# Kernel tuning notes

Hardware: AMD Instinct MI355X
Metric: run time of the kernel (lower is better)

The kernel has to match this reference:

```python
import jax, jax.numpy as jnp
import numpy as np

N = 131072          # collocation points per dataset
C_WAVE = 1.0        # wave speed c
DIMS = [2, 256, 256, 256, 256, 1]


def _glorot(k, shape):
    fan_in, fan_out = shape
    std = jnp.sqrt(2.0 / (fan_in + fan_out)).astype(jnp.float32)
    return std * jax.random.normal(k, shape, dtype=jnp.float32)


def setup_inputs() -> dict:
    key = jax.random.key(0)
    ks = jax.random.split(key, 16)
    inp = {}
    for i in range(5):
        inp[f"W{i}"] = _glorot(ks[i], (DIMS[i], DIMS[i + 1]))
        inp[f"b{i}"] = jnp.zeros((DIMS[i + 1],), jnp.float32)
    inp["tx_equation"] = jax.random.uniform(ks[10], (N, 2), dtype=jnp.float32)
    inp["tx_init"] = jax.random.uniform(ks[11], (N, 2), dtype=jnp.float32)
    # initial condition points have t=0 in practice; values don't affect the math pattern
    inp["tx_init"] = inp["tx_init"].at[:, 0].set(0.0)
    inp["tx_bound"] = jax.random.uniform(ks[12], (N, 2), dtype=jnp.float32)
    return inp


def _mlp(params, tx):
    # tanh MLP: (..., 2) -> (..., 1)
    h = tx
    for W, b in params[:-1]:
        h = jnp.tanh(h @ W + b)
    W, b = params[-1]
    return h @ W + b


def reference(W0, b0, W1, b1, W2, b2, W3, b3, W4, b4,
              tx_equation, tx_init, tx_bound):
    params = [(W0, b0), (W1, b1), (W2, b2), (W3, b3), (W4, b4)]

    def u_scalar(tx):  # tx: (2,) -> scalar u(t, x)
        return _mlp(params, tx[None, :])[0, 0]

    # PDE residual: u_tt - c^2 * u_xx via per-point Hessian diagonal (input_diagonal_hessian)
    hess = jax.vmap(jax.hessian(u_scalar))(tx_equation)      # (N, 2, 2)
    u_tt = hess[:, 0, 0]
    u_xx = hess[:, 1, 1]
    pde_residual = (u_tt - (C_WAVE ** 2) * u_xx)[:, None]     # (N, 1)

    # Initial conditions: u and du/dt (input_gradient)
    u_init, g = jax.vmap(jax.value_and_grad(u_scalar))(tx_init)  # (N,), (N, 2)
    u_phi = u_init[:, None]                                   # (N, 1)
    du_dt_psi = g[:, 0][:, None]                              # (N, 1)

    # Boundary: plain forward
    u_bound = _mlp(params, tx_bound)                          # (N, 1)

    return jnp.stack([pde_residual, u_phi, du_dt_psi, u_bound], axis=0)  # (4, N, 1)
```

## Files before the change

### kernel.cpp

```cpp
#include <hip/hip_runtime.h>
#include <math.h>

#define N_PTS 131072
#define HID   256

typedef __attribute__((ext_vector_type(8)))  _Float16 f16x8;
typedef __attribute__((ext_vector_type(4)))  float    f32x4;
typedef __attribute__((ext_vector_type(16))) float    f32x16;
typedef unsigned int u32;
typedef __attribute__((address_space(1))) const u32 gu32;
typedef __attribute__((address_space(3))) u32       lu32;

#define LDS_HI  0
#define LDS_W   32768
#define LDS_SZ  49152

__device__ __forceinline__ int act_off(int row, int kbyte) {
    return row * 512 + (kbyte ^ ((row & 7) << 4));
}
__device__ __forceinline__ void tanh_f1(float z, float& h, float& f1) {
    float s = __expf(2.0f * z);
    float r = __builtin_amdgcn_rcpf(s + 1.0f);
    h  = fmaf(-2.0f, r, 1.0f);
    f1 = (1.0f - h) * (1.0f + h);
}

__global__ void prep_w(const float* __restrict__ W1, const float* __restrict__ W2,
                       const float* __restrict__ W3, char* __restrict__ ws)
{
    int idx = blockIdx.x * 256 + threadIdx.x;
    int l = idx >> 16;
    int e = idx & 65535;
    int k = e >> 8, n = e & 255;
    const float* W = (l == 0) ? W1 : (l == 1) ? W2 : W3;
    float w = W[e];
    int slab = l * 16 + (k >> 4);
    int byte_in = ((k >> 3) & 1) * 4096 + n * 16 + (k & 7) * 2;
    *(_Float16*)(ws + (size_t)slab * 8192 + byte_in) = (_Float16)w;
}

__device__ __forceinline__ void stage_slab(const char* __restrict__ src,
                                           char* dst, int tid) {
    #pragma unroll
    for (int q = 0; q < 2; ++q) {
        __builtin_amdgcn_global_load_lds((gu32*)(src + q * 4096 + tid * 16),
                                         (lu32*)(dst + q * 4096 + tid * 16), 16, 0, 0);
    }
}

template<int S, int PTS>
__global__ void __launch_bounds__(256, 3)
pinn_mfma(const float* __restrict__ W0, const float* __restrict__ b0,
          const float* __restrict__ b1, const float* __restrict__ b2,
          const float* __restrict__ b3,
          const float* __restrict__ W4, const float* __restrict__ b4,
          const char* __restrict__ wpre,
          const float* __restrict__ tx, float* __restrict__ out)
{
    extern __shared__ char lds[];
    const int tid  = threadIdx.x;
    const int lane = tid & 63;
    const int wid  = tid >> 6;
    const int pbase = blockIdx.x * PTS;
    constexpr int CG = 256 / PTS;
    constexpr int NC = 256 / CG;
    const int ep  = tid / CG;
    const int ec0 = (tid % CG) * NC;

    stage_slab(wpre, lds + LDS_W, tid);

    {
        const float tt = tx[2 * (pbase + ep) + 0];
        const float xx = tx[2 * (pbase + ep) + 1];
        for (int cb = ec0; cb < ec0 + NC; cb += 8) {
            alignas(16) float w0r[8], w1r[8], bb[8];
            *(f32x4*)&w0r[0] = *(const f32x4*)(W0 + cb);
            *(f32x4*)&w0r[4] = *(const f32x4*)(W0 + cb + 4);
            *(f32x4*)&w1r[0] = *(const f32x4*)(W0 + HID + cb);
            *(f32x4*)&w1r[4] = *(const f32x4*)(W0 + HID + cb + 4);
            *(f32x4*)&bb[0]  = *(const f32x4*)(b0 + cb);
            *(f32x4*)&bb[4]  = *(const f32x4*)(b0 + cb + 4);
            f16x8 vhi[S];
            #pragma unroll
            for (int j = 0; j < 8; ++j) {
                float z = fmaf(tt, w0r[j], fmaf(xx, w1r[j], bb[j]));
                float h, f1;
                tanh_f1(z, h, f1);
                vhi[0][j] = (_Float16)h;
                if (S == 2) {
                    vhi[1][j] = (_Float16)(f1 * w0r[j]);
                } else if (S == 4) {
                    float d1 = w0r[j] + w1r[j];
                    float d2 = w0r[j] - w1r[j];
                    float f2 = -2.0f * h * f1;
                    vhi[1][j] = (_Float16)(f1 * d1);
                    vhi[2][j] = (_Float16)(f1 * d2);
                    vhi[3][j] = (_Float16)(f2 * d1 * d2);
                }
            }
            #pragma unroll
            for (int s2 = 0; s2 < S; ++s2) {
                int row = ep * S + s2;
                *(f16x8*)(lds + LDS_HI + act_off(row, cb * 2)) = vhi[s2];
            }
        }
    }

    const int c0 = wid * 64 + (lane & 31);
    float bcv[3][2];
    bcv[0][0] = b1[c0]; bcv[0][1] = b1[c0 + 32];
    bcv[1][0] = b2[c0]; bcv[1][1] = b2[c0 + 32];
    bcv[2][0] = b3[c0]; bcv[2][1] = b3[c0 + 32];

    asm volatile("s_waitcnt vmcnt(0) lgkmcnt(0)" ::: "memory");
    __builtin_amdgcn_sched_barrier(0);
    __builtin_amdgcn_s_barrier();
    __builtin_amdgcn_sched_barrier(0);

    #pragma unroll
    for (int l = 0; l < 3; ++l) {
        f32x16 acc[2][2];
        #pragma unroll
        for (int i = 0; i < 2; ++i)
            #pragma unroll
            for (int j = 0; j < 2; ++j)
                acc[i][j] = (f32x16){0.f,0.f,0.f,0.f,0.f,0.f,0.f,0.f,
                                     0.f,0.f,0.f,0.f,0.f,0.f,0.f,0.f};

        #pragma unroll
        for (int ph = 0; ph < 16; ++ph) {
            const int g = l * 16 + ph;
            if (ph > 0) {
                asm volatile("s_waitcnt vmcnt(0)" ::: "memory");
                __builtin_amdgcn_s_barrier();
                __builtin_amdgcn_sched_barrier(0);
            }
            if (g < 47) {
                stage_slab(wpre + (size_t)(g + 1) * 8192,
                           lds + LDS_W + ((g + 1) & 1) * 8192, tid);
            }
            const int kbyte = ph * 32 + ((lane >> 5) << 4);
            f16x8 av[2], bv[2];
            #pragma unroll
            for (int i = 0; i < 2; ++i) {
                const int row = i * 32 + (lane & 31);
                av[i] = *(const f16x8*)(lds + LDS_HI + act_off(row, kbyte));
            }
            const char* wb = lds + LDS_W + (g & 1) * 8192 + ((lane >> 5) << 12);
            #pragma unroll
            for (int j = 0; j < 2; ++j) {
                const int n = wid * 64 + j * 32 + (lane & 31);
                bv[j] = *(const f16x8*)(wb + n * 16);
            }
            __builtin_amdgcn_s_setprio(1);
            acc[0][0] = __builtin_amdgcn_mfma_f32_32x32x16_f16(av[0], bv[0], acc[0][0], 0, 0, 0);
            acc[0][1] = __builtin_amdgcn_mfma_f32_32x32x16_f16(av[0], bv[1], acc[0][1], 0, 0, 0);
            acc[1][0] = __builtin_amdgcn_mfma_f32_32x32x16_f16(av[1], bv[0], acc[1][0], 0, 0, 0);
            acc[1][1] = __builtin_amdgcn_mfma_f32_32x32x16_f16(av[1], bv[1], acc[1][1], 0, 0, 0);
            __builtin_amdgcn_s_setprio(0);
        }
        __builtin_amdgcn_s_barrier();

        #pragma unroll
        for (int i = 0; i < 2; ++i) {
            #pragma unroll
            for (int j = 0; j < 2; ++j) {
                const int colj = wid * 64 + j * 32 + (lane & 31);
                const float bias = bcv[l][j];
                const int rtb = i * 32 + 4 * (lane >> 5);
                #pragma unroll
                for (int q = 0; q < 4; ++q) {
                    const int rb = rtb + 8 * q;
                    if (S == 4) {
                        float z0 = acc[i][j][4*q+0] + bias;
                        float z1 = acc[i][j][4*q+1];
                        float z2 = acc[i][j][4*q+2];
                        float zm = acc[i][j][4*q+3];
                        float h, f1;
                        tanh_f1(z0, h, f1);
                        float f2 = -2.0f * h * f1;
                        *(_Float16*)(lds + LDS_HI + act_off(rb+0, colj*2)) = (_Float16)h;
                        *(_Float16*)(lds + LDS_HI + act_off(rb+1, colj*2)) = (_Float16)(f1 * z1);
                        *(_Float16*)(lds + LDS_HI + act_off(rb+2, colj*2)) = (_Float16)(f1 * z2);
                        *(_Float16*)(lds + LDS_HI + act_off(rb+3, colj*2)) =
                            (_Float16)(fmaf(f1, zm, f2 * z1 * z2));
                    } else if (S == 2) {
                        #pragma unroll
                        for (int pp = 0; pp < 2; ++pp) {
                            float z0 = acc[i][j][4*q+2*pp+0] + bias;
                            float zd = acc[i][j][4*q+2*pp+1];
                            float h, f1;
                            tanh_f1(z0, h, f1);
                            *(_Float16*)(lds + LDS_HI + act_off(rb+2*pp+0, colj*2)) = (_Float16)h;
                            *(_Float16*)(lds + LDS_HI + act_off(rb+2*pp+1, colj*2)) = (_Float16)(f1 * zd);
                        }
                    } else {
                        #pragma unroll
                        for (int m = 0; m < 4; ++m) {
                            float z0 = acc[i][j][4*q+m] + bias;
                            float h, f1;
                            tanh_f1(z0, h, f1);
                            *(_Float16*)(lds + LDS_HI + act_off(rb+m, colj*2)) = (_Float16)h;
                        }
                    }
                }
            }
        }
        asm volatile("s_waitcnt vmcnt(0) lgkmcnt(0)" ::: "memory");
        __builtin_amdgcn_sched_barrier(0);
        __builtin_amdgcn_s_barrier();
        __builtin_amdgcn_sched_barrier(0);
    }

    if (S == 4) {
        const int p   = tid >> 4;
        const int seg = tid & 15;
        const int k0  = seg * 16;
        const int row = 4 * p + 3;
        float d = 0.0f;
        #pragma unroll
        for (int kb = 0; kb < 16; kb += 8) {
            f16x8 h8 = *(const f16x8*)(lds + LDS_HI + act_off(row, (k0 + kb) * 2));
            alignas(16) float wv[8];
            *(f32x4*)&wv[0] = *(const f32x4*)(W4 + k0 + kb);
            *(f32x4*)&wv[4] = *(const f32x4*)(W4 + k0 + kb + 4);
            #pragma unroll
            for (int j = 0; j < 8; ++j) d = fmaf((float)h8[j], wv[j], d);
        }
        #pragma unroll
        for (int off = 8; off > 0; off >>= 1) d += __shfl_down(d, off, 16);
        if (seg == 0) out[0 * N_PTS + pbase + p] = d;
    } else {
        const int row = tid >> 2;
        const int seg = tid & 3;
        const int k0  = seg * 64;
        float d = 0.0f;
        #pragma unroll
        for (int kb = 0; kb < 64; kb += 8) {
            f16x8 h8 = *(const f16x8*)(lds + LDS_HI + act_off(row, (k0 + kb) * 2));
            alignas(16) float wv[8];
            *(f32x4*)&wv[0] = *(const f32x4*)(W4 + k0 + kb);
            *(f32x4*)&wv[4] = *(const f32x4*)(W4 + k0 + kb + 4);
            #pragma unroll
            for (int j = 0; j < 8; ++j) d = fmaf((float)h8[j], wv[j], d);
        }
        d += __shfl_down(d, 2, 4);
        d += __shfl_down(d, 1, 4);
        if (seg == 0) {
            if (S == 2) {
                const int p = row >> 1;
                if ((row & 1) == 0) out[1 * N_PTS + pbase + p] = d + b4[0];
                else                out[2 * N_PTS + pbase + p] = d;
            } else {
                out[3 * N_PTS + pbase + row] = d + b4[0];
            }
        }
    }
}

extern "C" void kernel_launch(void* const* d_in, const int* in_sizes, int n_in,
                              void* d_out, int out_size, void* d_ws, size_t ws_size,
                              hipStream_t stream) {
    const float* W0 = (const float*)d_in[0];
    const float* b0 = (const float*)d_in[1];
    const float* W1 = (const float*)d_in[2];
    const float* b1 = (const float*)d_in[3];
    const float* W2 = (const float*)d_in[4];
    const float* b2 = (const float*)d_in[5];
    const float* W3 = (const float*)d_in[6];
    const float* b3 = (const float*)d_in[7];
    const float* W4 = (const float*)d_in[8];
    const float* b4 = (const float*)d_in[9];
    const float* tx_eq    = (const float*)d_in[10];
    const float* tx_init  = (const float*)d_in[11];
    const float* tx_bound = (const float*)d_in[12];
    float* out = (float*)d_out;
    char* wpre = (char*)d_ws;

    prep_w<<<768, 256, 0, stream>>>(W1, W2, W3, wpre);
    pinn_mfma<4,16><<<N_PTS/16, 256, LDS_SZ, stream>>>(W0,b0,b1,b2,b3,W4,b4,wpre,tx_eq,   out);
    pinn_mfma<2,32><<<N_PTS/32, 256, LDS_SZ, stream>>>(W0,b0,b1,b2,b3,W4,b4,wpre,tx_init, out);
    pinn_mfma<1,64><<<N_PTS/64, 256, LDS_SZ, stream>>>(W0,b0,b1,b2,b3,W4,b4,wpre,tx_bound,out);
}
```

Measured before the change: 563.7 us.

## Load MFMA weight operands directly from global into registers, drop LDS weight staging

Weights are now laid out per output column with K contiguous and fetched straight from global/L2 into registers, using a three-deep register prefetch ring. Activations use a padded LDS row stride in place of the XOR swizzle and are prefetched two steps ahead. This removes the per-slab LDS staging and the 16 block barriers per layer, and cuts LDS to about 33KB, which may allow more resident blocks. In exchange every wave issues its own global loads for weights, so the loop depends on L2 latency and bandwidth rather than shared reuse in LDS.

```diff
diff --git a/kernel.cpp b/kernel.cpp
--- a/kernel.cpp
+++ b/kernel.cpp
@@ -3,21 +3,12 @@
 
 #define N_PTS 131072
 #define HID   256
+#define P_ACT 528
 
 typedef __attribute__((ext_vector_type(8)))  _Float16 f16x8;
 typedef __attribute__((ext_vector_type(4)))  float    f32x4;
 typedef __attribute__((ext_vector_type(16))) float    f32x16;
-typedef unsigned int u32;
-typedef __attribute__((address_space(1))) const u32 gu32;
-typedef __attribute__((address_space(3))) u32       lu32;
-
-#define LDS_HI  0
-#define LDS_W   32768
-#define LDS_SZ  49152
-
-__device__ __forceinline__ int act_off(int row, int kbyte) {
-    return row * 512 + (kbyte ^ ((row & 7) << 4));
-}
+
 __device__ __forceinline__ void tanh_f1(float z, float& h, float& f1) {
     float s = __expf(2.0f * z);
     float r = __builtin_amdgcn_rcpf(s + 1.0f);
@@ -33,19 +24,7 @@
     int e = idx & 65535;
     int k = e >> 8, n = e & 255;
     const float* W = (l == 0) ? W1 : (l == 1) ? W2 : W3;
-    float w = W[e];
-    int slab = l * 16 + (k >> 4);
-    int byte_in = ((k >> 3) & 1) * 4096 + n * 16 + (k & 7) * 2;
-    *(_Float16*)(ws + (size_t)slab * 8192 + byte_in) = (_Float16)w;
-}
-
-__device__ __forceinline__ void stage_slab(const char* __restrict__ src,
-                                           char* dst, int tid) {
-    #pragma unroll
-    for (int q = 0; q < 2; ++q) {
-        __builtin_amdgcn_global_load_lds((gu32*)(src + q * 4096 + tid * 16),
-                                         (lu32*)(dst + q * 4096 + tid * 16), 16, 0, 0);
-    }
+    *(_Float16*)(ws + (size_t)l * 131072 + n * 512 + k * 2) = (_Float16)W[e];
 }
 
 template<int S, int PTS>
@@ -57,17 +36,17 @@
           const char* __restrict__ wpre,
           const float* __restrict__ tx, float* __restrict__ out)
 {
-    extern __shared__ char lds[];
+    __shared__ char act[64 * P_ACT];
     const int tid  = threadIdx.x;
     const int lane = tid & 63;
     const int wid  = tid >> 6;
+    const int l31  = lane & 31;
+    const int h16  = (lane >> 5) << 4;
     const int pbase = blockIdx.x * PTS;
     constexpr int CG = 256 / PTS;
     constexpr int NC = 256 / CG;
     const int ep  = tid / CG;
     const int ec0 = (tid % CG) * NC;
-
-    stage_slab(wpre, lds + LDS_W, tid);
 
     {
         const float tt = tx[2 * (pbase + ep) + 0];
@@ -101,24 +80,31 @@
             #pragma unroll
             for (int s2 = 0; s2 < S; ++s2) {
                 int row = ep * S + s2;
-                *(f16x8*)(lds + LDS_HI + act_off(row, cb * 2)) = vhi[s2];
+                *(f16x8*)(act + row * P_ACT + cb * 2) = vhi[s2];
             }
         }
     }
 
-    const int c0 = wid * 64 + (lane & 31);
+    const int c0 = wid * 64 + l31;
     float bcv[3][2];
     bcv[0][0] = b1[c0]; bcv[0][1] = b1[c0 + 32];
     bcv[1][0] = b2[c0]; bcv[1][1] = b2[c0 + 32];
     bcv[2][0] = b3[c0]; bcv[2][1] = b3[c0 + 32];
 
-    asm volatile("s_waitcnt vmcnt(0) lgkmcnt(0)" ::: "memory");
+    asm volatile("s_waitcnt lgkmcnt(0)" ::: "memory");
     __builtin_amdgcn_sched_barrier(0);
     __builtin_amdgcn_s_barrier();
     __builtin_amdgcn_sched_barrier(0);
 
+    const char* aA[2];
+    aA[0] = act + (0 * 32 + l31) * P_ACT + h16;
+    aA[1] = act + (1 * 32 + l31) * P_ACT + h16;
+
     #pragma unroll
     for (int l = 0; l < 3; ++l) {
+        const char* gB0 = wpre + (size_t)l * 131072 + (wid * 64 +      l31) * 512 + h16;
+        const char* gB1 = wpre + (size_t)l * 131072 + (wid * 64 + 32 + l31) * 512 + h16;
+
         f32x16 acc[2][2];
         #pragma unroll
         for (int i = 0; i < 2; ++i)
@@ -127,50 +113,51 @@
                 acc[i][j] = (f32x16){0.f,0.f,0.f,0.f,0.f,0.f,0.f,0.f,
                                      0.f,0.f,0.f,0.f,0.f,0.f,0.f,0.f};
 
+        f16x8 br[3][2], ar[2][2];
+        #pragma unroll
+        for (int f = 0; f < 3; ++f) {
+            br[f][0] = *(const f16x8*)(gB0 + f * 32);
+            br[f][1] = *(const f16x8*)(gB1 + f * 32);
+        }
+        #pragma unroll
+        for (int f = 0; f < 2; ++f) {
+            ar[f][0] = *(const f16x8*)(aA[0] + f * 32);
+            ar[f][1] = *(const f16x8*)(aA[1] + f * 32);
+        }
+
         #pragma unroll
         for (int ph = 0; ph < 16; ++ph) {
-            const int g = l * 16 + ph;
-            if (ph > 0) {
-                asm volatile("s_waitcnt vmcnt(0)" ::: "memory");
-                __builtin_amdgcn_s_barrier();
-                __builtin_amdgcn_sched_barrier(0);
-            }
-            if (g < 47) {
-                stage_slab(wpre + (size_t)(g + 1) * 8192,
-                           lds + LDS_W + ((g + 1) & 1) * 8192, tid);
-            }
-            const int kbyte = ph * 32 + ((lane >> 5) << 4);
-            f16x8 av[2], bv[2];
-            #pragma unroll
-            for (int i = 0; i < 2; ++i) {
-                const int row = i * 32 + (lane & 31);
-                av[i] = *(const f16x8*)(lds + LDS_HI + act_off(row, kbyte));
-            }
-            const char* wb = lds + LDS_W + (g & 1) * 8192 + ((lane >> 5) << 12);
+            const int bs = ph % 3;
+            const int as = ph % 2;
+            __builtin_amdgcn_s_setprio(1);
+            acc[0][0] = __builtin_amdgcn_mfma_f32_32x32x16_f16(ar[as][0], br[bs][0], acc[0][0], 0, 0, 0);
+            acc[0][1] = __builtin_amdgcn_mfma_f32_32x32x16_f16(ar[as][0], br[bs][1], acc[0][1], 0, 0, 0);
+            acc[1][0] = __builtin_amdgcn_mfma_f32_32x32x16_f16(ar[as][1], br[bs][0], acc[1][0], 0, 0, 0);
+            acc[1][1] = __builtin_amdgcn_mfma_f32_32x32x16_f16(ar[as][1], br[bs][1], acc[1][1], 0, 0, 0);
+            __builtin_amdgcn_s_setprio(0);
+            if (ph + 3 < 16) {
+                br[bs][0] = *(const f16x8*)(gB0 + (ph + 3) * 32);
+                br[bs][1] = *(const f16x8*)(gB1 + (ph + 3) * 32);
+            }
+            if (ph + 2 < 16) {
+                ar[as][0] = *(const f16x8*)(aA[0] + (ph + 2) * 32);
+                ar[as][1] = *(const f16x8*)(aA[1] + (ph + 2) * 32);
+            }
+        }
+
+        __builtin_amdgcn_s_barrier();
+
+        #pragma unroll
+        for (int i = 0; i < 2; ++i) {
             #pragma unroll
             for (int j = 0; j < 2; ++j) {
-                const int n = wid * 64 + j * 32 + (lane & 31);
-                bv[j] = *(const f16x8*)(wb + n * 16);
-            }
-            __builtin_amdgcn_s_setprio(1);
-            acc[0][0] = __builtin_amdgcn_mfma_f32_32x32x16_f16(av[0], bv[0], acc[0][0], 0, 0, 0);
-            acc[0][1] = __builtin_amdgcn_mfma_f32_32x32x16_f16(av[0], bv[1], acc[0][1], 0, 0, 0);
-            acc[1][0] = __builtin_amdgcn_mfma_f32_32x32x16_f16(av[1], bv[0], acc[1][0], 0, 0, 0);
-            acc[1][1] = __builtin_amdgcn_mfma_f32_32x32x16_f16(av[1], bv[1], acc[1][1], 0, 0, 0);
-            __builtin_amdgcn_s_setprio(0);
-        }
-        __builtin_amdgcn_s_barrier();
-
-        #pragma unroll
-        for (int i = 0; i < 2; ++i) {
-            #pragma unroll
-            for (int j = 0; j < 2; ++j) {
-                const int colj = wid * 64 + j * 32 + (lane & 31);
+                const int colj = wid * 64 + j * 32 + l31;
                 const float bias = bcv[l][j];
                 const int rtb = i * 32 + 4 * (lane >> 5);
+                char* eb = act + rtb * P_ACT + colj * 2;
                 #pragma unroll
                 for (int q = 0; q < 4; ++q) {
-                    const int rb = rtb + 8 * q;
+                    const int ro = 8 * q * P_ACT;
                     if (S == 4) {
                         float z0 = acc[i][j][4*q+0] + bias;
                         float z1 = acc[i][j][4*q+1];
@@ -179,11 +166,10 @@
                         float h, f1;
                         tanh_f1(z0, h, f1);
                         float f2 = -2.0f * h * f1;
-                        *(_Float16*)(lds + LDS_HI + act_off(rb+0, colj*2)) = (_Float16)h;
-                        *(_Float16*)(lds + LDS_HI + act_off(rb+1, colj*2)) = (_Float16)(f1 * z1);
-                        *(_Float16*)(lds + LDS_HI + act_off(rb+2, colj*2)) = (_Float16)(f1 * z2);
-                        *(_Float16*)(lds + LDS_HI + act_off(rb+3, colj*2)) =
-                            (_Float16)(fmaf(f1, zm, f2 * z1 * z2));
+                        *(_Float16*)(eb + ro)             = (_Float16)h;
+                        *(_Float16*)(eb + ro + P_ACT)     = (_Float16)(f1 * z1);
+                        *(_Float16*)(eb + ro + 2 * P_ACT) = (_Float16)(f1 * z2);
+                        *(_Float16*)(eb + ro + 3 * P_ACT) = (_Float16)(fmaf(f1, zm, f2 * z1 * z2));
                     } else if (S == 2) {
                         #pragma unroll
                         for (int pp = 0; pp < 2; ++pp) {
@@ -191,8 +177,8 @@
                             float zd = acc[i][j][4*q+2*pp+1];
                             float h, f1;
                             tanh_f1(z0, h, f1);
-                            *(_Float16*)(lds + LDS_HI + act_off(rb+2*pp+0, colj*2)) = (_Float16)h;
-                            *(_Float16*)(lds + LDS_HI + act_off(rb+2*pp+1, colj*2)) = (_Float16)(f1 * zd);
+                            *(_Float16*)(eb + ro + (2*pp) * P_ACT)     = (_Float16)h;
+                            *(_Float16*)(eb + ro + (2*pp + 1) * P_ACT) = (_Float16)(f1 * zd);
                         }
                     } else {
                         #pragma unroll
@@ -200,13 +186,13 @@
                             float z0 = acc[i][j][4*q+m] + bias;
                             float h, f1;
                             tanh_f1(z0, h, f1);
-                            *(_Float16*)(lds + LDS_HI + act_off(rb+m, colj*2)) = (_Float16)h;
+                            *(_Float16*)(eb + ro + m * P_ACT) = (_Float16)h;
                         }
                     }
                 }
             }
         }
-        asm volatile("s_waitcnt vmcnt(0) lgkmcnt(0)" ::: "memory");
+        asm volatile("s_waitcnt lgkmcnt(0)" ::: "memory");
         __builtin_amdgcn_sched_barrier(0);
         __builtin_amdgcn_s_barrier();
         __builtin_amdgcn_sched_barrier(0);
@@ -220,7 +206,7 @@
         float d = 0.0f;
         #pragma unroll
         for (int kb = 0; kb < 16; kb += 8) {
-            f16x8 h8 = *(const f16x8*)(lds + LDS_HI + act_off(row, (k0 + kb) * 2));
+            f16x8 h8 = *(const f16x8*)(act + row * P_ACT + (k0 + kb) * 2);
             alignas(16) float wv[8];
             *(f32x4*)&wv[0] = *(const f32x4*)(W4 + k0 + kb);
             *(f32x4*)&wv[4] = *(const f32x4*)(W4 + k0 + kb + 4);
@@ -237,7 +223,7 @@
         float d = 0.0f;
         #pragma unroll
         for (int kb = 0; kb < 64; kb += 8) {
-            f16x8 h8 = *(const f16x8*)(lds + LDS_HI + act_off(row, (k0 + kb) * 2));
+            f16x8 h8 = *(const f16x8*)(act + row * P_ACT + (k0 + kb) * 2);
             alignas(16) float wv[8];
             *(f32x4*)&wv[0] = *(const f32x4*)(W4 + k0 + kb);
             *(f32x4*)&wv[4] = *(const f32x4*)(W4 + k0 + kb + 4);
@@ -278,7 +264,7 @@
     char* wpre = (char*)d_ws;
 
     prep_w<<<768, 256, 0, stream>>>(W1, W2, W3, wpre);
-    pinn_mfma<4,16><<<N_PTS/16, 256, LDS_SZ, stream>>>(W0,b0,b1,b2,b3,W4,b4,wpre,tx_eq,   out);
-    pinn_mfma<2,32><<<N_PTS/32, 256, LDS_SZ, stream>>>(W0,b0,b1,b2,b3,W4,b4,wpre,tx_init, out);
-    pinn_mfma<1,64><<<N_PTS/64, 256, LDS_SZ, stream>>>(W0,b0,b1,b2,b3,W4,b4,wpre,tx_bound,out);
-}
+    pinn_mfma<4,16><<<N_PTS/16, 256, 0, stream>>>(W0,b0,b1,b2,b3,W4,b4,wpre,tx_eq,   out);
+    pinn_mfma<2,32><<<N_PTS/32, 256, 0, stream>>>(W0,b0,b1,b2,b3,W4,b4,wpre,tx_init, out);
+    pinn_mfma<1,64><<<N_PTS/64, 256, 0, stream>>>(W0,b0,b1,b2,b3,W4,b4,wpre,tx_bound,out);
+}
```

New measurement: 771.0 us. 36.8% more time.

## Use per-wave triple-buffered weight staging with fewer block barriers

Applied to the files above, without the earlier changes.

Weight slabs are repacked so each wave stages only its own 64-column slice of B into a private triple-buffered LDS region. A K-chunk grows to 32, and the per-slab block-wide barrier is replaced by per-wave vmcnt waits, halving the phase count and removing most s_barriers in the GEMM loop. The activation swizzle changes from XOR to a rotate. LDS grows to 80KB and launch bounds drop to 2 blocks per CU, trading occupancy for deeper prefetch and less synchronisation.

```diff
diff --git a/kernel.cpp b/kernel.cpp
--- a/kernel.cpp
+++ b/kernel.cpp
@@ -11,12 +11,12 @@
 typedef __attribute__((address_space(1))) const u32 gu32;
 typedef __attribute__((address_space(3))) u32       lu32;
 
-#define LDS_HI  0
-#define LDS_W   32768
-#define LDS_SZ  49152
-
-__device__ __forceinline__ int act_off(int row, int kbyte) {
-    return row * 512 + (kbyte ^ ((row & 7) << 4));
+#define LDS_ACT 0
+#define LDS_B   32768
+#define LDS_SZ  81920
+
+__device__ __forceinline__ int act_addr(int row, int kbyte) {
+    return row * 512 + ((kbyte + ((row & 31) << 4)) & 511);
 }
 __device__ __forceinline__ void tanh_f1(float z, float& h, float& f1) {
     float s = __expf(2.0f * z);
@@ -34,22 +34,24 @@
     int k = e >> 8, n = e & 255;
     const float* W = (l == 0) ? W1 : (l == 1) ? W2 : W3;
     float w = W[e];
-    int slab = l * 16 + (k >> 4);
-    int byte_in = ((k >> 3) & 1) * 4096 + n * 16 + (k & 7) * 2;
-    *(_Float16*)(ws + (size_t)slab * 8192 + byte_in) = (_Float16)w;
-}
-
-__device__ __forceinline__ void stage_slab(const char* __restrict__ src,
-                                           char* dst, int tid) {
+    int kc = k >> 5, ks = (k >> 4) & 1, h = (k >> 3) & 1;
+    size_t base = (size_t)(((l * 8 + kc) * 4) + (n >> 6)) * 4096;
+    int byte_in = (ks * 2 + h) * 1024 + (n & 63) * 16 + (k & 7) * 2;
+    *(_Float16*)(ws + base + byte_in) = (_Float16)w;
+}
+
+__device__ __forceinline__ void stage_b(const char* __restrict__ wpre, char* ldsB,
+                                        int g, int wid, int lane) {
+    const char* src = wpre + (size_t)(g * 4 + wid) * 4096 + lane * 16;
+    char* dst = ldsB + wid * 12288 + (g % 3) * 4096 + lane * 16;
     #pragma unroll
-    for (int q = 0; q < 2; ++q) {
-        __builtin_amdgcn_global_load_lds((gu32*)(src + q * 4096 + tid * 16),
-                                         (lu32*)(dst + q * 4096 + tid * 16), 16, 0, 0);
-    }
+    for (int q = 0; q < 4; ++q)
+        __builtin_amdgcn_global_load_lds((gu32*)(src + q * 1024),
+                                         (lu32*)(dst + q * 1024), 16, 0, 0);
 }
 
 template<int S, int PTS>
-__global__ void __launch_bounds__(256, 3)
+__global__ void __launch_bounds__(256, 2)
 pinn_mfma(const float* __restrict__ W0, const float* __restrict__ b0,
           const float* __restrict__ b1, const float* __restrict__ b2,
           const float* __restrict__ b3,
@@ -61,13 +63,14 @@
     const int tid  = threadIdx.x;
     const int lane = tid & 63;
     const int wid  = tid >> 6;
+    const int l31  = lane & 31;
+    const int hh   = lane >> 5;
+    const int h16  = hh << 4;
     const int pbase = blockIdx.x * PTS;
     constexpr int CG = 256 / PTS;
     constexpr int NC = 256 / CG;
     const int ep  = tid / CG;
     const int ec0 = (tid % CG) * NC;
-
-    stage_slab(wpre, lds + LDS_W, tid);
 
     {
         const float tt = tx[2 * (pbase + ep) + 0];
@@ -101,18 +104,21 @@
             #pragma unroll
             for (int s2 = 0; s2 < S; ++s2) {
                 int row = ep * S + s2;
-                *(f16x8*)(lds + LDS_HI + act_off(row, cb * 2)) = vhi[s2];
+                *(f16x8*)(lds + LDS_ACT + act_addr(row, cb * 2)) = vhi[s2];
             }
         }
     }
 
-    const int c0 = wid * 64 + (lane & 31);
+    const int c0 = wid * 64 + l31;
     float bcv[3][2];
     bcv[0][0] = b1[c0]; bcv[0][1] = b1[c0 + 32];
     bcv[1][0] = b2[c0]; bcv[1][1] = b2[c0 + 32];
     bcv[2][0] = b3[c0]; bcv[2][1] = b3[c0 + 32];
 
-    asm volatile("s_waitcnt vmcnt(0) lgkmcnt(0)" ::: "memory");
+    __builtin_amdgcn_sched_barrier(0);
+    stage_b(wpre, lds + LDS_B, 0, wid, lane);
+    stage_b(wpre, lds + LDS_B, 1, wid, lane);
+    asm volatile("s_waitcnt vmcnt(8) lgkmcnt(0)" ::: "memory");
     __builtin_amdgcn_sched_barrier(0);
     __builtin_amdgcn_s_barrier();
     __builtin_amdgcn_sched_barrier(0);
@@ -128,46 +134,41 @@
                                      0.f,0.f,0.f,0.f,0.f,0.f,0.f,0.f};
 
         #pragma unroll
-        for (int ph = 0; ph < 16; ++ph) {
-            const int g = l * 16 + ph;
-            if (ph > 0) {
-                asm volatile("s_waitcnt vmcnt(0)" ::: "memory");
-                __builtin_amdgcn_s_barrier();
-                __builtin_amdgcn_sched_barrier(0);
-            }
-            if (g < 47) {
-                stage_slab(wpre + (size_t)(g + 1) * 8192,
-                           lds + LDS_W + ((g + 1) & 1) * 8192, tid);
-            }
-            const int kbyte = ph * 32 + ((lane >> 5) << 4);
-            f16x8 av[2], bv[2];
-            #pragma unroll
-            for (int i = 0; i < 2; ++i) {
-                const int row = i * 32 + (lane & 31);
-                av[i] = *(const f16x8*)(lds + LDS_HI + act_off(row, kbyte));
-            }
-            const char* wb = lds + LDS_W + (g & 1) * 8192 + ((lane >> 5) << 12);
+        for (int ph = 0; ph < 8; ++ph) {
+            const int g = l * 8 + ph;
+            if (g == 23) { asm volatile("s_waitcnt vmcnt(0)" ::: "memory"); }
+            else         { asm volatile("s_waitcnt vmcnt(4)" ::: "memory"); }
+            __builtin_amdgcn_sched_barrier(0);
+            if (g < 22) stage_b(wpre, lds + LDS_B, g + 2, wid, lane);
+
+            const char* bslab = lds + LDS_B + wid * 12288 + (g % 3) * 4096 + hh * 1024;
+            #pragma unroll
+            for (int ks = 0; ks < 2; ++ks) {
+                const int kbyte = ph * 64 + ks * 32 + h16;
+                f16x8 av[2], bv[2];
+                #pragma unroll
+                for (int i = 0; i < 2; ++i)
+                    av[i] = *(const f16x8*)(lds + LDS_ACT + act_addr(i * 32 + l31, kbyte));
+                #pragma unroll
+                for (int j = 0; j < 2; ++j)
+                    bv[j] = *(const f16x8*)(bslab + ks * 2048 + j * 512 + l31 * 16);
+                __builtin_amdgcn_s_setprio(1);
+                acc[0][0] = __builtin_amdgcn_mfma_f32_32x32x16_f16(av[0], bv[0], acc[0][0], 0, 0, 0);
+                acc[0][1] = __builtin_amdgcn_mfma_f32_32x32x16_f16(av[0], bv[1], acc[0][1], 0, 0, 0);
+                acc[1][0] = __builtin_amdgcn_mfma_f32_32x32x16_f16(av[1], bv[0], acc[1][0], 0, 0, 0);
+                acc[1][1] = __builtin_amdgcn_mfma_f32_32x32x16_f16(av[1], bv[1], acc[1][1], 0, 0, 0);
+                __builtin_amdgcn_s_setprio(0);
+            }
+        }
+        __builtin_amdgcn_s_barrier();
+
+        #pragma unroll
+        for (int i = 0; i < 2; ++i) {
             #pragma unroll
             for (int j = 0; j < 2; ++j) {
-                const int n = wid * 64 + j * 32 + (lane & 31);
-                bv[j] = *(const f16x8*)(wb + n * 16);
-            }
-            __builtin_amdgcn_s_setprio(1);
-            acc[0][0] = __builtin_amdgcn_mfma_f32_32x32x16_f16(av[0], bv[0], acc[0][0], 0, 0, 0);
-            acc[0][1] = __builtin_amdgcn_mfma_f32_32x32x16_f16(av[0], bv[1], acc[0][1], 0, 0, 0);
-            acc[1][0] = __builtin_amdgcn_mfma_f32_32x32x16_f16(av[1], bv[0], acc[1][0], 0, 0, 0);
-            acc[1][1] = __builtin_amdgcn_mfma_f32_32x32x16_f16(av[1], bv[1], acc[1][1], 0, 0, 0);
-            __builtin_amdgcn_s_setprio(0);
-        }
-        __builtin_amdgcn_s_barrier();
-
-        #pragma unroll
-        for (int i = 0; i < 2; ++i) {
-            #pragma unroll
-            for (int j = 0; j < 2; ++j) {
-                const int colj = wid * 64 + j * 32 + (lane & 31);
+                const int colj = wid * 64 + j * 32 + l31;
                 const float bias = bcv[l][j];
-                const int rtb = i * 32 + 4 * (lane >> 5);
+                const int rtb = i * 32 + 4 * hh;
                 #pragma unroll
                 for (int q = 0; q < 4; ++q) {
                     const int rb = rtb + 8 * q;
@@ -179,10 +180,10 @@
                         float h, f1;
                         tanh_f1(z0, h, f1);
                         float f2 = -2.0f * h * f1;
-                        *(_Float16*)(lds + LDS_HI + act_off(rb+0, colj*2)) = (_Float16)h;
-                        *(_Float16*)(lds + LDS_HI + act_off(rb+1, colj*2)) = (_Float16)(f1 * z1);
-                        *(_Float16*)(lds + LDS_HI + act_off(rb+2, colj*2)) = (_Float16)(f1 * z2);
-                        *(_Float16*)(lds + LDS_HI + act_off(rb+3, colj*2)) =
+                        *(_Float16*)(lds + LDS_ACT + act_addr(rb+0, colj*2)) = (_Float16)h;
+                        *(_Float16*)(lds + LDS_ACT + act_addr(rb+1, colj*2)) = (_Float16)(f1 * z1);
+                        *(_Float16*)(lds + LDS_ACT + act_addr(rb+2, colj*2)) = (_Float16)(f1 * z2);
+                        *(_Float16*)(lds + LDS_ACT + act_addr(rb+3, colj*2)) =
                             (_Float16)(fmaf(f1, zm, f2 * z1 * z2));
                     } else if (S == 2) {
                         #pragma unroll
@@ -191,8 +192,8 @@
                             float zd = acc[i][j][4*q+2*pp+1];
                             float h, f1;
                             tanh_f1(z0, h, f1);
-                            *(_Float16*)(lds + LDS_HI + act_off(rb+2*pp+0, colj*2)) = (_Float16)h;
-                            *(_Float16*)(lds + LDS_HI + act_off(rb+2*pp+1, colj*2)) = (_Float16)(f1 * zd);
+                            *(_Float16*)(lds + LDS_ACT + act_addr(rb+2*pp+0, colj*2)) = (_Float16)h;
+                            *(_Float16*)(lds + LDS_ACT + act_addr(rb+2*pp+1, colj*2)) = (_Float16)(f1 * zd);
                         }
                     } else {
                         #pragma unroll
@@ -200,13 +201,13 @@
                             float z0 = acc[i][j][4*q+m] + bias;
                             float h, f1;
                             tanh_f1(z0, h, f1);
-                            *(_Float16*)(lds + LDS_HI + act_off(rb+m, colj*2)) = (_Float16)h;
+                            *(_Float16*)(lds + LDS_ACT + act_addr(rb+m, colj*2)) = (_Float16)h;
                         }
                     }
                 }
             }
         }
-        asm volatile("s_waitcnt vmcnt(0) lgkmcnt(0)" ::: "memory");
+        asm volatile("s_waitcnt lgkmcnt(0)" ::: "memory");
         __builtin_amdgcn_sched_barrier(0);
         __builtin_amdgcn_s_barrier();
         __builtin_amdgcn_sched_barrier(0);
@@ -220,7 +221,7 @@
         float d = 0.0f;
         #pragma unroll
         for (int kb = 0; kb < 16; kb += 8) {
-            f16x8 h8 = *(const f16x8*)(lds + LDS_HI + act_off(row, (k0 + kb) * 2));
+            f16x8 h8 = *(const f16x8*)(lds + LDS_ACT + act_addr(row, (k0 + kb) * 2));
             alignas(16) float wv[8];
             *(f32x4*)&wv[0] = *(const f32x4*)(W4 + k0 + kb);
             *(f32x4*)&wv[4] = *(const f32x4*)(W4 + k0 + kb + 4);
@@ -237,7 +238,7 @@
         float d = 0.0f;
         #pragma unroll
         for (int kb = 0; kb < 64; kb += 8) {
-            f16x8 h8 = *(const f16x8*)(lds + LDS_HI + act_off(row, (k0 + kb) * 2));
+            f16x8 h8 = *(const f16x8*)(lds + LDS_ACT + act_addr(row, (k0 + kb) * 2));
             alignas(16) float wv[8];
             *(f32x4*)&wv[0] = *(const f32x4*)(W4 + k0 + kb);
             *(f32x4*)&wv[4] = *(const f32x4*)(W4 + k0 + kb + 4);
@@ -277,6 +278,10 @@
     float* out = (float*)d_out;
     char* wpre = (char*)d_ws;
 
+    hipFuncSetAttribute((const void*)pinn_mfma<4,16>, hipFuncAttributeMaxDynamicSharedMemorySize, LDS_SZ);
+    hipFuncSetAttribute((const void*)pinn_mfma<2,32>, hipFuncAttributeMaxDynamicSharedMemorySize, LDS_SZ);
+    hipFuncSetAttribute((const void*)pinn_mfma<1,64>, hipFuncAttributeMaxDynamicSharedMemorySize, LDS_SZ);
+
     prep_w<<<768, 256, 0, stream>>>(W1, W2, W3, wpre);
     pinn_mfma<4,16><<<N_PTS/16, 256, LDS_SZ, stream>>>(W0,b0,b1,b2,b3,W4,b4,wpre,tx_eq,   out);
     pinn_mfma<2,32><<<N_PTS/32, 256, LDS_SZ, stream>>>(W0,b0,b1,b2,b3,W4,b4,wpre,tx_init, out);
```

Measured after the change: 586.8 us. 1.04x slower.
